# Kernel optimization log

Hardware: AMD Instinct MI355X
Metric: run time of the kernel (lower is better)

The kernel has to match this reference:

```python
import jax, jax.numpy as jnp
import numpy as np

N = 50000
E = 1600000
F_IN = 128
MP_UNITS = [32, 32, 32, 32, 16, 16, 16, 16, 8, 8, 8, 8]
MLP_UNITS = [16, 16]
DELTA = 2.0


def _lin(k, fi, fo):
    kw, kb = jax.random.split(k)
    s = 1.0 / np.sqrt(fi)
    W = jax.random.uniform(kw, (fi, fo), minval=-s, maxval=s, dtype=jnp.float32)
    b = jax.random.uniform(kb, (fo,), minval=-s, maxval=s, dtype=jnp.float32)
    return W, b


def setup_inputs() -> dict:
    key = jax.random.key(0)
    ks = jax.random.split(key, 64)
    inp = {}
    inp['x'] = jax.random.normal(ks[0], (N, F_IN), dtype=jnp.float32)
    inp['edge_index'] = jax.random.randint(ks[1], (2, E), 0, N, dtype=jnp.int32)
    inp['edge_weight'] = jax.random.uniform(ks[2], (E,), dtype=jnp.float32)
    inp['Wi'], inp['bi'] = _lin(ks[3], F_IN, F_IN)
    d = F_IN
    for i, u in enumerate(MP_UNITS):
        inp['Wc%d' % i], inp['bc%d' % i] = _lin(ks[4 + i], d, u)
        d = u
    for i, u in enumerate(MLP_UNITS):
        inp['Wm%d' % i], inp['bm%d' % i] = _lin(ks[20 + i], d, u)
        d = u
    inp['Wf'], inp['bf'] = _lin(ks[30], d, 1)
    return inp


def reference(x, edge_index, edge_weight, Wi, bi,
              Wc0, bc0, Wc1, bc1, Wc2, bc2, Wc3, bc3, Wc4, bc4, Wc5, bc5,
              Wc6, bc6, Wc7, bc7, Wc8, bc8, Wc9, bc9, Wc10, bc10, Wc11, bc11,
              Wm0, bm0, Wm1, bm1, Wf, bf):
    n = x.shape[0]
    src, dst = edge_index[0], edge_index[1]
    # delta_gcn_matrix: P = (1-delta) I + delta * D^{-1/2} A D^{-1/2}
    deg = jax.ops.segment_sum(edge_weight, dst, num_segments=n)
    dinv = jnp.where(deg > 0, jax.lax.rsqrt(jnp.maximum(deg, 1e-12)), 0.0)
    w = DELTA * dinv[src] * edge_weight * dinv[dst]  # [E]
    self_w = 1.0 - DELTA

    h = x @ Wi + bi

    def conv(h, W, b):
        hw = h @ W                                        # [N, out]
        msg = hw[src] * w[:, None]                        # gather + scale [E, out]
        agg = jax.ops.segment_sum(msg, dst, num_segments=n)  # scatter-add
        return agg + self_w * hw + b                      # fold in self-loops

    convs = [(Wc0, bc0), (Wc1, bc1), (Wc2, bc2), (Wc3, bc3), (Wc4, bc4), (Wc5, bc5),
             (Wc6, bc6), (Wc7, bc7), (Wc8, bc8), (Wc9, bc9), (Wc10, bc10), (Wc11, bc11)]
    for W, b in convs:
        h = jnp.tanh(conv(h, W, b))
    for W, b in [(Wm0, bm0), (Wm1, bm1)]:
        h = jax.nn.relu(h @ W + b)
    return jnp.tanh(h @ Wf + bf)  # [N, 1]
```

## Files before the change

### kernel.cpp

```cpp
#include <hip/hip_runtime.h>


constexpr int kN = 50000;
constexpr int kE = 1600000;
constexpr float kSelfW = -1.0f;
constexpr int kCAP = 72;
constexpr int PAD_N = 50176;
constexpr int kPROWS = PAD_N / 8;
constexpr int E4  = kE / 4;
constexpr int E8B = (E4 + 511) / 512;
constexpr int NBG = (kN + 255) / 256;

typedef int      v4i __attribute__((ext_vector_type(4)));
typedef float    v4f __attribute__((ext_vector_type(4)));
typedef _Float16 h8v __attribute__((ext_vector_type(8)));

__device__ __forceinline__ int rowmap(int r) {
  return (r & 7) * kPROWS + (r >> 3);
}
__device__ __forceinline__ unsigned packcw(int colMapped, float w) {
  _Float16 h = (_Float16)w;
  unsigned short u;
  __builtin_memcpy(&u, &h, 2);
  return (unsigned)(unsigned short)colMapped | ((unsigned)u << 16);
}
__device__ __forceinline__ float unpw(unsigned e) {
  unsigned short u = (unsigned short)(e >> 16);
  _Float16 h;
  __builtin_memcpy(&h, &u, 2);
  return (float)h;
}
__device__ __forceinline__ unsigned pack2h(float a, float b) {
  _Float16 ha = (_Float16)a, hb = (_Float16)b;
  unsigned short ua, ub;
  __builtin_memcpy(&ua, &ha, 2);
  __builtin_memcpy(&ub, &hb, 2);
  return (unsigned)ua | ((unsigned)ub << 16);
}
__device__ __forceinline__ float fast_tanh(float x) {
  float t = __expf(2.0f * x);
  float r = __builtin_amdgcn_rcpf(t + 1.0f);
  return 1.0f - 2.0f * r;
}

__global__ __launch_bounds__(256)
void prep(int* __restrict__ cnt, const float* __restrict__ Wi,
          const float* __restrict__ bi, const float* __restrict__ Wc0,
          float* __restrict__ Weff, float* __restrict__ beff) {
  if (blockIdx.x < 49) {
    int i = blockIdx.x * 1024 + threadIdx.x * 4;
    *reinterpret_cast<int4*>(cnt + i) = make_int4(0, 0, 0, 0);
  } else {
    int idx = (blockIdx.x - 49) * 256 + threadIdx.x;
    if (idx >= 129 * 32) return;
    int r = idx >> 5, j = idx & 31;
    float acc = 0.0f;
    if (r < 128) {
      for (int k = 0; k < 128; ++k) acc += Wi[r * 128 + k] * Wc0[k * 32 + j];
      Weff[r * 32 + j] = acc;
    } else {
      for (int k = 0; k < 128; ++k) acc += bi[k] * Wc0[k * 32 + j];
      beff[j] = acc;
    }
  }
}

__global__ __launch_bounds__(256)
void build_cnt_gemm0(const int* __restrict__ src, const int* __restrict__ dst,
                     const float* __restrict__ ew, int* __restrict__ cnt,
                     unsigned* __restrict__ ecw,
                     const float* __restrict__ X,
                     const float* __restrict__ Weff,
                     const float* __restrict__ beff,
                     _Float16* __restrict__ Y, int e4, int n) {
  __shared__ unsigned s_buf[4128];
  if (blockIdx.x < NBG) {
    float* smem = reinterpret_cast<float*>(s_buf);
    for (int idx = threadIdx.x; idx < 128 * 32; idx += 256) {
      int j = idx >> 7, k = idx & 127;
      smem[j * 128 + k] = Weff[k * 32 + j];
    }
    if (threadIdx.x < 32) smem[4096 + threadIdx.x] = beff[threadIdx.x];
    __syncthreads();
    int row = blockIdx.x * 256 + threadIdx.x;
    if (row >= n) return;
    float acc[32];
#pragma unroll
    for (int j = 0; j < 32; ++j) acc[j] = smem[4096 + j];
    const float4* xr = reinterpret_cast<const float4*>(X + (size_t)row * 128);
    const float4* Ws4 = reinterpret_cast<const float4*>(smem);
    for (int k4 = 0; k4 < 32; ++k4) {
      float4 a = xr[k4];
#pragma unroll
      for (int j = 0; j < 32; ++j) {
        float4 wv = Ws4[j * 32 + k4];
        acc[j] += a.x * wv.x + a.y * wv.y + a.z * wv.z + a.w * wv.w;
      }
    }
    h8v* yr = reinterpret_cast<h8v*>(Y + (size_t)rowmap(row) * 32);
#pragma unroll
    for (int j8 = 0; j8 < 4; ++j8) {
      h8v v;
#pragma unroll
      for (int q = 0; q < 8; ++q) v[q] = (_Float16)acc[8 * j8 + q];
      yr[j8] = v;
    }
    return;
  }
  unsigned*       s_cw = s_buf;
  unsigned short* s_br = reinterpret_cast<unsigned short*>(s_buf + 2048);
  int*            s_cnt = reinterpret_cast<int*>(s_buf + 3072);
  if (threadIdx.x == 0) *s_cnt = 0;
  __syncthreads();
  int b = blockIdx.x - NBG;
  int p = blockIdx.x & 7;
  int chunk = b >> 3;
  int lane = threadIdx.x & 63;
  int i0 = chunk * 512 + threadIdx.x;
  int i1 = i0 + 256;
  v4i svA = {0,0,0,0}, dvA = {-1,-1,-1,-1};
  v4i svB = {0,0,0,0}, dvB = {-1,-1,-1,-1};
  v4f wvA = {0,0,0,0}, wvB = {0,0,0,0};
  bool vA = i0 < e4, vB = i1 < e4;
  if (vA) {
    svA = reinterpret_cast<const v4i*>(src)[i0];
    dvA = reinterpret_cast<const v4i*>(dst)[i0];
    wvA = reinterpret_cast<const v4f*>(ew)[i0];
  }
  if (vB) {
    svB = reinterpret_cast<const v4i*>(src)[i1];
    dvB = reinterpret_cast<const v4i*>(dst)[i1];
    wvB = reinterpret_cast<const v4f*>(ew)[i1];
  }
#pragma unroll
  for (int g = 0; g < 2; ++g) {
    v4i sv = g ? svB : svA;
    v4i dv = g ? dvB : dvA;
    v4f wv = g ? wvB : wvA;
    bool valid = g ? vB : vA;
#pragma unroll
    for (int c = 0; c < 4; ++c) {
      bool keep = valid && ((dv[c] & 7) == p);
      unsigned long long mask = __ballot(keep);
      int base = 0;
      int nb = __popcll(mask);
      if (lane == 0 && nb) base = atomicAdd(s_cnt, nb);
      base = __shfl(base, 0, 64);
      if (keep) {
        int pos = base + __popcll(mask & ((1ull << lane) - 1ull));
        s_cw[pos] = packcw(rowmap(sv[c]), wv[c]);
        s_br[pos] = (unsigned short)(dv[c] >> 3);
      }
    }
  }
  __syncthreads();
  int m = *s_cnt;
  for (int t = threadIdx.x; t < m; t += 256) {
    int br = p * kPROWS + s_br[t];
    int r = atomicAdd(&cnt[br], 1);
    if (r < kCAP) ecw[(size_t)br * kCAP + r] = s_cw[t];
  }
}

__global__ __launch_bounds__(256)
void deg_dinv_wave(const int* __restrict__ cnt, const unsigned* __restrict__ ecw,
                   float* __restrict__ dinv) {
  int lane = threadIdx.x & 63;
  int br = blockIdx.x * 4 + (threadIdx.x >> 6);
  int deg = min(cnt[br], kCAP);
  size_t base = (size_t)br * kCAP;
  float d = 0.0f;
  for (int i = lane; i < deg; i += 64) d += unpw(ecw[base + i]);
#pragma unroll
  for (int off = 32; off > 0; off >>= 1) d += __shfl_xor(d, off, 64);
  if (lane == 0) dinv[br] = (d > 0.0f) ? rsqrtf(fmaxf(d, 1e-12f)) : 0.0f;
}

__global__ __launch_bounds__(256)
void wscale_wave(const int* __restrict__ cnt, unsigned* __restrict__ ecw,
                 const float* __restrict__ dinv) {
  int lane = threadIdx.x & 63;
  int br = blockIdx.x * 4 + (threadIdx.x >> 6);
  int deg = min(cnt[br], kCAP);
  size_t base = (size_t)br * kCAP;
  float dr = 2.0f * dinv[br];
  for (int i = lane; i < kCAP; i += 64) {
    if (i < deg) {
      unsigned e = ecw[base + i];
      int cm = e & 0xFFFFu;
      ecw[base + i] = packcw(cm, dr * dinv[cm] * unpw(e));
    } else {
      ecw[base + i] = 0u;
    }
  }
}

template <int DOUT, int DNEXT, bool FINAL>
__global__ __launch_bounds__(256)
void spmm_fused(const _Float16* __restrict__ HW, const int* __restrict__ cnt,
                const unsigned* __restrict__ ecw, const float* __restrict__ b,
                const float* __restrict__ Wn, void* __restrict__ Out,
                const float* __restrict__ Wm0, const float* __restrict__ bm0,
                const float* __restrict__ Wm1, const float* __restrict__ bm1,
                const float* __restrict__ Wf, const float* __restrict__ bf,
                int n) {
  constexpr int R = 64 / DOUT;
  constexpr int W = DOUT;
  constexpr int L = DOUT / 8;
  constexpr int S = 8;
  constexpr int WST = DNEXT + 1;
  constexpr int JPT = (DNEXT > 0) ? (DNEXT / S) : 1;
  __shared__ float smem[(DNEXT > 0) ? DOUT * WST : 448];
  if constexpr (DNEXT > 0) {
    for (int idx = threadIdx.x; idx < DOUT * DNEXT; idx += 256) {
      int k = idx / DNEXT, j = idx - k * DNEXT;
      smem[k * WST + j] = Wn[idx];
    }
    __syncthreads();
  }
  if constexpr (FINAL) {
    int t = threadIdx.x;
    if (t < 128) smem[t] = Wm0[t];
    if (t < 256) smem[128 + t] = Wm1[t];
    if (t < 16) {
      smem[384 + t] = bm0[t];
      smem[400 + t] = bm1[t];
      smem[416 + t] = Wf[t];
    }
    if (t == 0) smem[432] = bf[0];
    __syncthreads();
  }
  int lane = threadIdx.x & 63;
  int wid = threadIdx.x >> 6;
  int g = lane / W;
  int gl = lane - g * W;
  int ch8 = gl & (L - 1);
  int sub = gl / L;
  int p = blockIdx.x & 7;
  int q = blockIdx.x >> 3;
  int brLocal = q * (4 * R) + wid * R + g;
  int br = p * kPROWS + brLocal;
  int deg = min(cnt[br], kCAP);
  const uint4* ecw4 = reinterpret_cast<const uint4*>(ecw + (size_t)br * kCAP);
  const h8v* HW8 = reinterpret_cast<const h8v*>(HW);
  uint4 ea = ecw4[sub];
  h8v a0 = HW8[(size_t)(ea.x & 0xFFFFu) * L + ch8];
  h8v a1 = HW8[(size_t)(ea.y & 0xFFFFu) * L + ch8];
  h8v a2 = HW8[(size_t)(ea.z & 0xFFFFu) * L + ch8];
  h8v a3 = HW8[(size_t)(ea.w & 0xFFFFu) * L + ch8];
  float wa0 = unpw(ea.x), wa1 = unpw(ea.y), wa2 = unpw(ea.z), wa3 = unpw(ea.w);
  float acc[8];
#pragma unroll
  for (int q8 = 0; q8 < 8; ++q8)
    acc[q8] = wa0 * (float)a0[q8] + wa1 * (float)a1[q8] +
              wa2 * (float)a2[q8] + wa3 * (float)a3[q8];
  if (deg > 32) {
    uint4 eb = ecw4[8 + sub];
    h8v b0 = HW8[(size_t)(eb.x & 0xFFFFu) * L + ch8];
    h8v b1 = HW8[(size_t)(eb.y & 0xFFFFu) * L + ch8];
    h8v b2 = HW8[(size_t)(eb.z & 0xFFFFu) * L + ch8];
    h8v b3 = HW8[(size_t)(eb.w & 0xFFFFu) * L + ch8];
    float wb0 = unpw(eb.x), wb1 = unpw(eb.y), wb2 = unpw(eb.z), wb3 = unpw(eb.w);
#pragma unroll
    for (int q8 = 0; q8 < 8; ++q8)
      acc[q8] += wb0 * (float)b0[q8] + wb1 * (float)b1[q8] +
                 wb2 * (float)b2[q8] + wb3 * (float)b3[q8];
    if (deg > 64) {
      if (sub < 2) {
        uint4 et = ecw4[16 + sub];
        h8v t0 = HW8[(size_t)(et.x & 0xFFFFu) * L + ch8];
        h8v t1 = HW8[(size_t)(et.y & 0xFFFFu) * L + ch8];
        h8v t2 = HW8[(size_t)(et.z & 0xFFFFu) * L + ch8];
        h8v t3 = HW8[(size_t)(et.w & 0xFFFFu) * L + ch8];
        float u0 = unpw(et.x), u1 = unpw(et.y), u2 = unpw(et.z), u3 = unpw(et.w);
#pragma unroll
        for (int q8 = 0; q8 < 8; ++q8)
          acc[q8] += u0 * (float)t0[q8] + u1 * (float)t1[q8] +
                     u2 * (float)t2[q8] + u3 * (float)t3[q8];
      }
    }
  }
#pragma unroll
  for (int off = W / 2; off >= L; off >>= 1) {
#pragma unroll
    for (int q8 = 0; q8 < 8; ++q8) acc[q8] += __shfl_xor(acc[q8], off, 64);
  }
  int krow = 8 * ch8;
  h8v hsv = HW8[(size_t)br * L + ch8];
  float h[8];
#pragma unroll
  for (int q8 = 0; q8 < 8; ++q8)
    h[q8] = fast_tanh(acc[q8] + kSelfW * (float)hsv[q8] + b[krow + q8]);
  if constexpr (FINAL) {
    int row = (brLocal << 3) | p;
    if (gl == 0 && row < n) {
      float y0[16];
#pragma unroll
      for (int j = 0; j < 16; ++j) {
        float v = smem[384 + j];
#pragma unroll
        for (int k = 0; k < 8; ++k) v += h[k] * smem[k * 16 + j];
        y0[j] = fmaxf(v, 0.0f);
      }
      float y1[16];
#pragma unroll
      for (int j = 0; j < 16; ++j) {
        float v = smem[400 + j];
#pragma unroll
        for (int k = 0; k < 16; ++k) v += y0[k] * smem[128 + k * 16 + j];
        y1[j] = fmaxf(v, 0.0f);
      }
      float z = smem[432];
#pragma unroll
      for (int k = 0; k < 16; ++k) z += y1[k] * smem[416 + k];
      reinterpret_cast<float*>(Out)[row] = fast_tanh(z);
    }
  } else {
    float pj[JPT];
    int jbase = sub * JPT;
#pragma unroll
    for (int jj = 0; jj < JPT; ++jj) {
      int j = jbase + jj;
      float v = 0.0f;
#pragma unroll
      for (int q8 = 0; q8 < 8; ++q8) v += h[q8] * smem[(krow + q8) * WST + j];
      pj[jj] = v;
    }
#pragma unroll
    for (int off = 1; off < L; off <<= 1) {
#pragma unroll
      for (int jj = 0; jj < JPT; ++jj) pj[jj] += __shfl_xor(pj[jj], off, 64);
    }
    if (ch8 == 0) {
      _Float16* op = reinterpret_cast<_Float16*>(Out) + (size_t)br * DNEXT + jbase;
      if constexpr (JPT == 4) {
        uint2 u = make_uint2(pack2h(pj[0], pj[1]), pack2h(pj[2], pj[3]));
        *reinterpret_cast<uint2*>(op) = u;
      } else if constexpr (JPT == 2) {
        *reinterpret_cast<unsigned*>(op) = pack2h(pj[0], pj[1]);
      } else {
        op[0] = (_Float16)pj[0];
      }
    }
  }
}

extern "C" void kernel_launch(void* const* d_in, const int* in_sizes, int n_in,
                              void* d_out, int out_size, void* d_ws, size_t ws_size,
                              hipStream_t stream) {
  const float* x   = (const float*)d_in[0];
  const int*  eidx = (const int*)d_in[1];
  const float* ew  = (const float*)d_in[2];
  const float* Wi  = (const float*)d_in[3];
  const float* bi  = (const float*)d_in[4];
  const float* Wc[12]; const float* bc[12];
  for (int i = 0; i < 12; ++i) {
    Wc[i] = (const float*)d_in[5 + 2 * i];
    bc[i] = (const float*)d_in[6 + 2 * i];
  }
  const float* Wm0 = (const float*)d_in[29]; const float* bm0 = (const float*)d_in[30];
  const float* Wm1 = (const float*)d_in[31]; const float* bm1 = (const float*)d_in[32];
  const float* Wf  = (const float*)d_in[33]; const float* bf  = (const float*)d_in[34];
  float* out = (float*)d_out;

  const int* src = eidx;
  const int* dst = eidx + kE;

  float* wsf = (float*)d_ws;
  size_t off = 0;
  float*     dinv = wsf + off;              off += PAD_N;
  float*     Weff = wsf + off;              off += 128 * 32;
  float*     beff = wsf + off;              off += 64;
  int*       cnt  = (int*)(wsf + off);      off += PAD_N;
  unsigned*  ecw  = (unsigned*)(wsf + off); off += (size_t)PAD_N * kCAP;
  _Float16*  B16  = (_Float16*)(wsf + off); off += (size_t)PAD_N * 16;
  _Float16*  C16  = (_Float16*)(wsf + off); off += (size_t)PAD_N * 16;

  const int dgb  = PAD_N / 4;
  const int sb32 = PAD_N / 8;
  const int sb16 = PAD_N / 16;
  const int sb8  = PAD_N / 32;

  prep<<<66, 256, 0, stream>>>(cnt, Wi, bi, Wc[0], Weff, beff);
  build_cnt_gemm0<<<NBG + 8 * E8B, 256, 0, stream>>>(src, dst, ew, cnt, ecw,
                                                     x, Weff, beff, B16, E4, kN);
  deg_dinv_wave<<<dgb, 256, 0, stream>>>(cnt, ecw, dinv);
  wscale_wave<<<dgb, 256, 0, stream>>>(cnt, ecw, dinv);

  spmm_fused<32, 32, false><<<sb32, 256, 0, stream>>>(B16, cnt, ecw, bc[0], Wc[1], C16, nullptr, nullptr, nullptr, nullptr, nullptr, nullptr, kN);
  spmm_fused<32, 32, false><<<sb32, 256, 0, stream>>>(C16, cnt, ecw, bc[1], Wc[2], B16, nullptr, nullptr, nullptr, nullptr, nullptr, nullptr, kN);
  spmm_fused<32, 32, false><<<sb32, 256, 0, stream>>>(B16, cnt, ecw, bc[2], Wc[3], C16, nullptr, nullptr, nullptr, nullptr, nullptr, nullptr, kN);
  spmm_fused<32, 16, false><<<sb32, 256, 0, stream>>>(C16, cnt, ecw, bc[3], Wc[4], B16, nullptr, nullptr, nullptr, nullptr, nullptr, nullptr, kN);
  spmm_fused<16, 16, false><<<sb16, 256, 0, stream>>>(B16, cnt, ecw, bc[4], Wc[5], C16, nullptr, nullptr, nullptr, nullptr, nullptr, nullptr, kN);
  spmm_fused<16, 16, false><<<sb16, 256, 0, stream>>>(C16, cnt, ecw, bc[5], Wc[6], B16, nullptr, nullptr, nullptr, nullptr, nullptr, nullptr, kN);
  spmm_fused<16, 16, false><<<sb16, 256, 0, stream>>>(B16, cnt, ecw, bc[6], Wc[7], C16, nullptr, nullptr, nullptr, nullptr, nullptr, nullptr, kN);
  spmm_fused<16, 8, false><<<sb16, 256, 0, stream>>>(C16, cnt, ecw, bc[7], Wc[8], B16, nullptr, nullptr, nullptr, nullptr, nullptr, nullptr, kN);
  spmm_fused<8, 8, false><<<sb8, 256, 0, stream>>>(B16, cnt, ecw, bc[8], Wc[9], C16, nullptr, nullptr, nullptr, nullptr, nullptr, nullptr, kN);
  spmm_fused<8, 8, false><<<sb8, 256, 0, stream>>>(C16, cnt, ecw, bc[9], Wc[10], B16, nullptr, nullptr, nullptr, nullptr, nullptr, nullptr, kN);
  spmm_fused<8, 8, false><<<sb8, 256, 0, stream>>>(B16, cnt, ecw, bc[10], Wc[11], C16, nullptr, nullptr, nullptr, nullptr, nullptr, nullptr, kN);
  spmm_fused<8, 0, true><<<sb8, 256, 0, stream>>>(C16, cnt, ecw, bc[11], nullptr, out, Wm0, bm0, Wm1, bm1, Wf, bf, kN);
}
```

Baseline: 448.4 us.

## Fuse edge weight normalization into first SpMM and prepack src/weight edges

Removes the separate wscale pass. The first SpMM layer now computes the normalized weight 2*dinv[dst]*dinv[src]*w on the fly and writes the scaled packed entries back into the ELL buffer for later layers. The prep kernel now packs src and weight into 32-bit words ahead of the bucketing kernel, so that kernel reads two streams instead of three. Prep also zeroes the whole ELL buffer, replacing the padding clear that wscale used to do. The cost is an extra 6.4MB write and read for the prepacked array, a full ELL zeroing pass, and extra dinv gathers plus writes in the first layer.

```diff
diff --git a/kernel.cpp b/kernel.cpp
--- a/kernel.cpp
+++ b/kernel.cpp
@@ -10,8 +10,13 @@
 constexpr int E4  = kE / 4;
 constexpr int E8B = (E4 + 511) / 512;
 constexpr int NBG = (kN + 255) / 256;
+constexpr int ZB  = (PAD_N * 73) / 1024;
+constexpr int PKB = (E4 + 255) / 256;
+constexpr int WFB = 17;
+constexpr int PREPG = ZB + PKB + WFB;
 
 typedef int      v4i __attribute__((ext_vector_type(4)));
+typedef unsigned v4u __attribute__((ext_vector_type(4)));
 typedef float    v4f __attribute__((ext_vector_type(4)));
 typedef _Float16 h8v __attribute__((ext_vector_type(8)));
 
@@ -46,12 +51,25 @@
 __global__ __launch_bounds__(256)
 void prep(int* __restrict__ cnt, const float* __restrict__ Wi,
           const float* __restrict__ bi, const float* __restrict__ Wc0,
-          float* __restrict__ Weff, float* __restrict__ beff) {
-  if (blockIdx.x < 49) {
-    int i = blockIdx.x * 1024 + threadIdx.x * 4;
+          float* __restrict__ Weff, float* __restrict__ beff,
+          const int* __restrict__ src, const float* __restrict__ ew,
+          unsigned* __restrict__ cwe) {
+  if (blockIdx.x < ZB) {
+    size_t i = (size_t)blockIdx.x * 1024 + threadIdx.x * 4;
     *reinterpret_cast<int4*>(cnt + i) = make_int4(0, 0, 0, 0);
+  } else if (blockIdx.x < ZB + PKB) {
+    int i = (blockIdx.x - ZB) * 256 + threadIdx.x;
+    if (i >= E4) return;
+    v4i s = reinterpret_cast<const v4i*>(src)[i];
+    v4f w = reinterpret_cast<const v4f*>(ew)[i];
+    v4u c;
+    c.x = packcw(rowmap(s.x), w.x);
+    c.y = packcw(rowmap(s.y), w.y);
+    c.z = packcw(rowmap(s.z), w.z);
+    c.w = packcw(rowmap(s.w), w.w);
+    reinterpret_cast<v4u*>(cwe)[i] = c;
   } else {
-    int idx = (blockIdx.x - 49) * 256 + threadIdx.x;
+    int idx = (blockIdx.x - ZB - PKB) * 256 + threadIdx.x;
     if (idx >= 129 * 32) return;
     int r = idx >> 5, j = idx & 31;
     float acc = 0.0f;
@@ -66,9 +84,8 @@
 }
 
 __global__ __launch_bounds__(256)
-void build_cnt_gemm0(const int* __restrict__ src, const int* __restrict__ dst,
-                     const float* __restrict__ ew, int* __restrict__ cnt,
-                     unsigned* __restrict__ ecw,
+void build_cnt_gemm0(const int* __restrict__ dst, const unsigned* __restrict__ cwe,
+                     int* __restrict__ cnt, unsigned* __restrict__ ecw,
                      const float* __restrict__ X,
                      const float* __restrict__ Weff,
                      const float* __restrict__ beff,
@@ -118,25 +135,21 @@
   int lane = threadIdx.x & 63;
   int i0 = chunk * 512 + threadIdx.x;
   int i1 = i0 + 256;
-  v4i svA = {0,0,0,0}, dvA = {-1,-1,-1,-1};
-  v4i svB = {0,0,0,0}, dvB = {-1,-1,-1,-1};
-  v4f wvA = {0,0,0,0}, wvB = {0,0,0,0};
+  v4i dvA = {-1,-1,-1,-1}, dvB = {-1,-1,-1,-1};
+  v4u cvA = {0,0,0,0},     cvB = {0,0,0,0};
   bool vA = i0 < e4, vB = i1 < e4;
   if (vA) {
-    svA = reinterpret_cast<const v4i*>(src)[i0];
     dvA = reinterpret_cast<const v4i*>(dst)[i0];
-    wvA = reinterpret_cast<const v4f*>(ew)[i0];
+    cvA = reinterpret_cast<const v4u*>(cwe)[i0];
   }
   if (vB) {
-    svB = reinterpret_cast<const v4i*>(src)[i1];
     dvB = reinterpret_cast<const v4i*>(dst)[i1];
-    wvB = reinterpret_cast<const v4f*>(ew)[i1];
+    cvB = reinterpret_cast<const v4u*>(cwe)[i1];
   }
 #pragma unroll
   for (int g = 0; g < 2; ++g) {
-    v4i sv = g ? svB : svA;
     v4i dv = g ? dvB : dvA;
-    v4f wv = g ? wvB : wvA;
+    v4u cv = g ? cvB : cvA;
     bool valid = g ? vB : vA;
 #pragma unroll
     for (int c = 0; c < 4; ++c) {
@@ -148,7 +161,7 @@
       base = __shfl(base, 0, 64);
       if (keep) {
         int pos = base + __popcll(mask & ((1ull << lane) - 1ull));
-        s_cw[pos] = packcw(rowmap(sv[c]), wv[c]);
+        s_cw[pos] = cv[c];
         s_br[pos] = (unsigned short)(dv[c] >> 3);
       }
     }
@@ -176,29 +189,11 @@
   if (lane == 0) dinv[br] = (d > 0.0f) ? rsqrtf(fmaxf(d, 1e-12f)) : 0.0f;
 }
 
-__global__ __launch_bounds__(256)
-void wscale_wave(const int* __restrict__ cnt, unsigned* __restrict__ ecw,
-                 const float* __restrict__ dinv) {
-  int lane = threadIdx.x & 63;
-  int br = blockIdx.x * 4 + (threadIdx.x >> 6);
-  int deg = min(cnt[br], kCAP);
-  size_t base = (size_t)br * kCAP;
-  float dr = 2.0f * dinv[br];
-  for (int i = lane; i < kCAP; i += 64) {
-    if (i < deg) {
-      unsigned e = ecw[base + i];
-      int cm = e & 0xFFFFu;
-      ecw[base + i] = packcw(cm, dr * dinv[cm] * unpw(e));
-    } else {
-      ecw[base + i] = 0u;
-    }
-  }
-}
-
-template <int DOUT, int DNEXT, bool FINAL>
+template <int DOUT, int DNEXT, bool FINAL, bool SC>
 __global__ __launch_bounds__(256)
 void spmm_fused(const _Float16* __restrict__ HW, const int* __restrict__ cnt,
-                const unsigned* __restrict__ ecw, const float* __restrict__ b,
+                unsigned* __restrict__ ecw, const float* __restrict__ dv,
+                const float* __restrict__ b,
                 const float* __restrict__ Wn, void* __restrict__ Out,
                 const float* __restrict__ Wm0, const float* __restrict__ bm0,
                 const float* __restrict__ Wm1, const float* __restrict__ bm1,
@@ -241,14 +236,26 @@
   int brLocal = q * (4 * R) + wid * R + g;
   int br = p * kPROWS + brLocal;
   int deg = min(cnt[br], kCAP);
-  const uint4* ecw4 = reinterpret_cast<const uint4*>(ecw + (size_t)br * kCAP);
+  uint4* ecw4 = reinterpret_cast<uint4*>(ecw + (size_t)br * kCAP);
   const h8v* HW8 = reinterpret_cast<const h8v*>(HW);
+  float dbr = 0.0f;
+  if constexpr (SC) dbr = 2.0f * dv[br];
   uint4 ea = ecw4[sub];
   h8v a0 = HW8[(size_t)(ea.x & 0xFFFFu) * L + ch8];
   h8v a1 = HW8[(size_t)(ea.y & 0xFFFFu) * L + ch8];
   h8v a2 = HW8[(size_t)(ea.z & 0xFFFFu) * L + ch8];
   h8v a3 = HW8[(size_t)(ea.w & 0xFFFFu) * L + ch8];
-  float wa0 = unpw(ea.x), wa1 = unpw(ea.y), wa2 = unpw(ea.z), wa3 = unpw(ea.w);
+  float wa0, wa1, wa2, wa3;
+  if constexpr (SC) {
+    wa0 = dbr * dv[ea.x & 0xFFFFu] * unpw(ea.x);
+    wa1 = dbr * dv[ea.y & 0xFFFFu] * unpw(ea.y);
+    wa2 = dbr * dv[ea.z & 0xFFFFu] * unpw(ea.z);
+    wa3 = dbr * dv[ea.w & 0xFFFFu] * unpw(ea.w);
+    ecw4[sub] = make_uint4(packcw(ea.x & 0xFFFFu, wa0), packcw(ea.y & 0xFFFFu, wa1),
+                           packcw(ea.z & 0xFFFFu, wa2), packcw(ea.w & 0xFFFFu, wa3));
+  } else {
+    wa0 = unpw(ea.x); wa1 = unpw(ea.y); wa2 = unpw(ea.z); wa3 = unpw(ea.w);
+  }
   float acc[8];
 #pragma unroll
   for (int q8 = 0; q8 < 8; ++q8)
@@ -260,7 +267,17 @@
     h8v b1 = HW8[(size_t)(eb.y & 0xFFFFu) * L + ch8];
     h8v b2 = HW8[(size_t)(eb.z & 0xFFFFu) * L + ch8];
     h8v b3 = HW8[(size_t)(eb.w & 0xFFFFu) * L + ch8];
-    float wb0 = unpw(eb.x), wb1 = unpw(eb.y), wb2 = unpw(eb.z), wb3 = unpw(eb.w);
+    float wb0, wb1, wb2, wb3;
+    if constexpr (SC) {
+      wb0 = dbr * dv[eb.x & 0xFFFFu] * unpw(eb.x);
+      wb1 = dbr * dv[eb.y & 0xFFFFu] * unpw(eb.y);
+      wb2 = dbr * dv[eb.z & 0xFFFFu] * unpw(eb.z);
+      wb3 = dbr * dv[eb.w & 0xFFFFu] * unpw(eb.w);
+      ecw4[8 + sub] = make_uint4(packcw(eb.x & 0xFFFFu, wb0), packcw(eb.y & 0xFFFFu, wb1),
+                                 packcw(eb.z & 0xFFFFu, wb2), packcw(eb.w & 0xFFFFu, wb3));
+    } else {
+      wb0 = unpw(eb.x); wb1 = unpw(eb.y); wb2 = unpw(eb.z); wb3 = unpw(eb.w);
+    }
 #pragma unroll
     for (int q8 = 0; q8 < 8; ++q8)
       acc[q8] += wb0 * (float)b0[q8] + wb1 * (float)b1[q8] +
@@ -272,7 +289,17 @@
         h8v t1 = HW8[(size_t)(et.y & 0xFFFFu) * L + ch8];
         h8v t2 = HW8[(size_t)(et.z & 0xFFFFu) * L + ch8];
         h8v t3 = HW8[(size_t)(et.w & 0xFFFFu) * L + ch8];
-        float u0 = unpw(et.x), u1 = unpw(et.y), u2 = unpw(et.z), u3 = unpw(et.w);
+        float u0, u1, u2, u3;
+        if constexpr (SC) {
+          u0 = dbr * dv[et.x & 0xFFFFu] * unpw(et.x);
+          u1 = dbr * dv[et.y & 0xFFFFu] * unpw(et.y);
+          u2 = dbr * dv[et.z & 0xFFFFu] * unpw(et.z);
+          u3 = dbr * dv[et.w & 0xFFFFu] * unpw(et.w);
+          ecw4[16 + sub] = make_uint4(packcw(et.x & 0xFFFFu, u0), packcw(et.y & 0xFFFFu, u1),
+                                      packcw(et.z & 0xFFFFu, u2), packcw(et.w & 0xFFFFu, u3));
+        } else {
+          u0 = unpw(et.x); u1 = unpw(et.y); u2 = unpw(et.z); u3 = unpw(et.w);
+        }
 #pragma unroll
         for (int q8 = 0; q8 < 8; ++q8)
           acc[q8] += u0 * (float)t0[q8] + u1 * (float)t1[q8] +
@@ -375,28 +402,28 @@
   unsigned*  ecw  = (unsigned*)(wsf + off); off += (size_t)PAD_N * kCAP;
   _Float16*  B16  = (_Float16*)(wsf + off); off += (size_t)PAD_N * 16;
   _Float16*  C16  = (_Float16*)(wsf + off); off += (size_t)PAD_N * 16;
+  unsigned*  cwe  = (unsigned*)(wsf + off); off += kE;
 
   const int dgb  = PAD_N / 4;
   const int sb32 = PAD_N / 8;
   const int sb16 = PAD_N / 16;
   const int sb8  = PAD_N / 32;
 
-  prep<<<66, 256, 0, stream>>>(cnt, Wi, bi, Wc[0], Weff, beff);
-  build_cnt_gemm0<<<NBG + 8 * E8B, 256, 0, stream>>>(src, dst, ew, cnt, ecw,
+  prep<<<PREPG, 256, 0, stream>>>(cnt, Wi, bi, Wc[0], Weff, beff, src, ew, cwe);
+  build_cnt_gemm0<<<NBG + 8 * E8B, 256, 0, stream>>>(dst, cwe, cnt, ecw,
                                                      x, Weff, beff, B16, E4, kN);
   deg_dinv_wave<<<dgb, 256, 0, stream>>>(cnt, ecw, dinv);
-  wscale_wave<<<dgb, 256, 0, stream>>>(cnt, ecw, dinv);
-
-  spmm_fused<32, 32, false><<<sb32, 256, 0, stream>>>(B16, cnt, ecw, bc[0], Wc[1], C16, nullptr, nullptr, nullptr, nullptr, nullptr, nullptr, kN);
-  spmm_fused<32, 32, false><<<sb32, 256, 0, stream>>>(C16, cnt, ecw, bc[1], Wc[2], B16, nullptr, nullptr, nullptr, nullptr, nullptr, nullptr, kN);
-  spmm_fused<32, 32, false><<<sb32, 256, 0, stream>>>(B16, cnt, ecw, bc[2], Wc[3], C16, nullptr, nullptr, nullptr, nullptr, nullptr, nullptr, kN);
-  spmm_fused<32, 16, false><<<sb32, 256, 0, stream>>>(C16, cnt, ecw, bc[3], Wc[4], B16, nullptr, nullptr, nullptr, nullptr, nullptr, nullptr, kN);
-  spmm_fused<16, 16, false><<<sb16, 256, 0, stream>>>(B16, cnt, ecw, bc[4], Wc[5], C16, nullptr, nullptr, nullptr, nullptr, nullptr, nullptr, kN);
-  spmm_fused<16, 16, false><<<sb16, 256, 0, stream>>>(C16, cnt, ecw, bc[5], Wc[6], B16, nullptr, nullptr, nullptr, nullptr, nullptr, nullptr, kN);
-  spmm_fused<16, 16, false><<<sb16, 256, 0, stream>>>(B16, cnt, ecw, bc[6], Wc[7], C16, nullptr, nullptr, nullptr, nullptr, nullptr, nullptr, kN);
-  spmm_fused<16, 8, false><<<sb16, 256, 0, stream>>>(C16, cnt, ecw, bc[7], Wc[8], B16, nullptr, nullptr, nullptr, nullptr, nullptr, nullptr, kN);
-  spmm_fused<8, 8, false><<<sb8, 256, 0, stream>>>(B16, cnt, ecw, bc[8], Wc[9], C16, nullptr, nullptr, nullptr, nullptr, nullptr, nullptr, kN);
-  spmm_fused<8, 8, false><<<sb8, 256, 0, stream>>>(C16, cnt, ecw, bc[9], Wc[10], B16, nullptr, nullptr, nullptr, nullptr, nullptr, nullptr, kN);
-  spmm_fused<8, 8, false><<<sb8, 256, 0, stream>>>(B16, cnt, ecw, bc[10], Wc[11], C16, nullptr, nullptr, nullptr, nullptr, nullptr, nullptr, kN);
-  spmm_fused<8, 0, true><<<sb8, 256, 0, stream>>>(C16, cnt, ecw, bc[11], nullptr, out, Wm0, bm0, Wm1, bm1, Wf, bf, kN);
-}
+
+  spmm_fused<32, 32, false, true ><<<sb32, 256, 0, stream>>>(B16, cnt, ecw, dinv, bc[0], Wc[1], C16, nullptr, nullptr, nullptr, nullptr, nullptr, nullptr, kN);
+  spmm_fused<32, 32, false, false><<<sb32, 256, 0, stream>>>(C16, cnt, ecw, dinv, bc[1], Wc[2], B16, nullptr, nullptr, nullptr, nullptr, nullptr, nullptr, kN);
+  spmm_fused<32, 32, false, false><<<sb32, 256, 0, stream>>>(B16, cnt, ecw, dinv, bc[2], Wc[3], C16, nullptr, nullptr, nullptr, nullptr, nullptr, nullptr, kN);
+  spmm_fused<32, 16, false, false><<<sb32, 256, 0, stream>>>(C16, cnt, ecw, dinv, bc[3], Wc[4], B16, nullptr, nullptr, nullptr, nullptr, nullptr, nullptr, kN);
+  spmm_fused<16, 16, false, false><<<sb16, 256, 0, stream>>>(B16, cnt, ecw, dinv, bc[4], Wc[5], C16, nullptr, nullptr, nullptr, nullptr, nullptr, nullptr, kN);
+  spmm_fused<16, 16, false, false><<<sb16, 256, 0, stream>>>(C16, cnt, ecw, dinv, bc[5], Wc[6], B16, nullptr, nullptr, nullptr, nullptr, nullptr, nullptr, kN);
+  spmm_fused<16, 16, false, false><<<sb16, 256, 0, stream>>>(B16, cnt, ecw, dinv, bc[6], Wc[7], C16, nullptr, nullptr, nullptr, nullptr, nullptr, nullptr, kN);
+  spmm_fused<16, 8, false, false><<<sb16, 256, 0, stream>>>(C16, cnt, ecw, dinv, bc[7], Wc[8], B16, nullptr, nullptr, nullptr, nullptr, nullptr, nullptr, kN);
+  spmm_fused<8, 8, false, false><<<sb8, 256, 0, stream>>>(B16, cnt, ecw, dinv, bc[8], Wc[9], C16, nullptr, nullptr, nullptr, nullptr, nullptr, nullptr, kN);
+  spmm_fused<8, 8, false, false><<<sb8, 256, 0, stream>>>(C16, cnt, ecw, dinv, bc[9], Wc[10], B16, nullptr, nullptr, nullptr, nullptr, nullptr, nullptr, kN);
+  spmm_fused<8, 8, false, false><<<sb8, 256, 0, stream>>>(B16, cnt, ecw, dinv, bc[10], Wc[11], C16, nullptr, nullptr, nullptr, nullptr, nullptr, nullptr, kN);
+  spmm_fused<8, 0, true, false><<<sb8, 256, 0, stream>>>(C16, cnt, ecw, dinv, bc[11], nullptr, out, Wm0, bm0, Wm1, bm1, Wf, bf, kN);
+}
```

New measurement: 449.0 us. About the same (+0.1%).
